# Kernel optimization log

Hardware: AMD Instinct MI355X
Metric: run time of the kernel (lower is better)

## Reference

```python
import jax, jax.numpy as jnp
import numpy as np

N = 100000      # nodes
E = 1600000     # edges (before self-loops)
DIN = 256
D = 128         # dmid == dout
L = 4           # n_layers
ALPHA = 0.5
THETA = 1.0
EPS = 1e-5      # pyg LayerNorm default eps


def setup_inputs() -> dict:
    key = jax.random.key(0)
    ks = jax.random.split(key, 6)
    x = jax.random.normal(ks[0], (N, DIN), jnp.float32)
    edge_index = jax.random.randint(ks[1], (2, E), 0, N)
    lin1_w = jax.random.normal(ks[2], (D, DIN), jnp.float32) * (1.0 / np.sqrt(DIN))
    lin1_b = jnp.zeros((D,), jnp.float32)
    w1 = jax.random.normal(ks[3], (L, D, D), jnp.float32) * (1.0 / np.sqrt(D))
    w2 = jax.random.normal(ks[4], (L, D, D), jnp.float32) * (1.0 / np.sqrt(D))
    norm_w = jnp.ones((D,), jnp.float32)
    norm_b = jnp.zeros((D,), jnp.float32)
    return {"x": x, "edge_index": edge_index, "lin1_w": lin1_w, "lin1_b": lin1_b,
            "w1": w1, "w2": w2, "norm_w": norm_w, "norm_b": norm_b}


def reference(x, edge_index, lin1_w, lin1_b, w1, w2, norm_w, norm_b):
    # --- gcn_norm: add self-loops, symmetric degree normalization ---
    sl = jnp.arange(N)
    row = jnp.concatenate([edge_index[0], sl])  # sources
    col = jnp.concatenate([edge_index[1], sl])  # targets (aggregation index)
    deg = jax.ops.segment_sum(jnp.ones(row.shape[0], jnp.float32), col, num_segments=N)
    dis = jax.lax.rsqrt(deg)  # deg >= 1 thanks to self-loops
    enorm = dis[row] * dis[col]  # [E+N]

    # --- f_0 = relu(lin1(x)); prev_h = 0 so x_0 arg == f_0 ---
    f0 = jax.nn.relu(x @ lin1_w.T + lin1_b)  # [N, D]
    x0 = ALPHA * f0
    f = f0

    for i in range(L):
        beta = float(np.log(THETA / (i + 1) + 1.0))
        # sparse neighbor aggregation: h = A_hat @ f
        h = jax.ops.segment_sum(f[row] * enorm[:, None], col, num_segments=N)
        h = h * (1.0 - ALPHA)
        # shared_weights=False: two separate identity/weight mixes
        out = ((1.0 - beta) * h + beta * (h @ w1[i])
               + (1.0 - beta) * x0 + beta * (x0 @ w2[i]))
        # pyg LayerNorm mode='graph', batch=None: normalize over all nodes+channels
        m = out.mean()
        s = jnp.sqrt(jnp.mean((out - m) ** 2))
        out = (out - m) / (s + EPS) * norm_w + norm_b
        f = jax.nn.relu(out)

    # dmid == dout -> lin2 is Identity
    return jax.nn.relu(f)
```

## Files before the change

kernel.cpp:

```cpp
#include <hip/hip_runtime.h>
#include <math.h>

constexpr int N    = 100000;
constexpr int E    = 1600000;
constexpr int DIN  = 256;
constexpr int D    = 128;
constexpr int L    = 4;
constexpr float EPS = 1e-5f;
constexpr int NPP  = 12500;

typedef __attribute__((ext_vector_type(8))) short bf16x8;
typedef __attribute__((ext_vector_type(4))) float f32x4;
typedef __attribute__((ext_vector_type(2))) float f32x2;

__device__ inline ushort f2b(float f) {
    uint u = __float_as_uint(f);
    uint r = u + 0x7fffu + ((u >> 16) & 1u);
    return (ushort)(r >> 16);
}
__device__ inline float b2f(ushort b) { return __uint_as_float(((uint)b) << 16); }


__global__ void k_count(const int* __restrict__ col, int* __restrict__ cnt) {
    int i = blockIdx.x * 256 + threadIdx.x;
    if (i * 2 + 1 < E) {
        int2 cc = ((const int2*)col)[i];
        atomicAdd(&cnt[cc.x], 1);
        atomicAdd(&cnt[cc.y], 1);
    } else if (i * 2 < E) {
        atomicAdd(&cnt[col[i * 2]], 1);
    }
}

__global__ void k_dis(const int* __restrict__ cnt, float* __restrict__ dis) {
    int n = blockIdx.x * 256 + threadIdx.x;
    if (n < N) dis[n] = rsqrtf((float)cnt[n] + 1.0f);
}

__global__ void k_blocksum(const int* __restrict__ cnt, int* __restrict__ bsum) {
    __shared__ int s[256];
    int base = blockIdx.x * 1024;
    int t = threadIdx.x;
    int a = 0;
    for (int j = 0; j < 4; j++) {
        int idx = base + t * 4 + j;
        if (idx < N) a += cnt[idx];
    }
    s[t] = a; __syncthreads();
    for (int off = 128; off > 0; off >>= 1) {
        if (t < off) s[t] += s[t + off];
        __syncthreads();
    }
    if (t == 0) bsum[blockIdx.x] = s[0];
}

__global__ void k_scan(int* __restrict__ bsum, int nb) {
    __shared__ int s[128];
    int t = threadIdx.x;
    int v = (t < nb) ? bsum[t] : 0;
    s[t] = v; __syncthreads();
    for (int off = 1; off < 128; off <<= 1) {
        int x = (t >= off) ? s[t - off] : 0;
        __syncthreads();
        s[t] += x;
        __syncthreads();
    }
    if (t < nb) bsum[t] = s[t] - v;
}

__global__ void k_offsets(const int* __restrict__ cnt, const int* __restrict__ bsum,
                          int* __restrict__ offs) {
    __shared__ int ls[256];
    int b = blockIdx.x, t = threadIdx.x;
    int base = b * 1024;
    int v[4]; int s = 0;
    for (int j = 0; j < 4; j++) {
        int idx = base + t * 4 + j;
        v[j] = (idx < N) ? cnt[idx] : 0;
        s += v[j];
    }
    ls[t] = s; __syncthreads();
    for (int off = 1; off < 256; off <<= 1) {
        int x = (t >= off) ? ls[t - off] : 0;
        __syncthreads();
        ls[t] += x;
        __syncthreads();
    }
    int excl = ((t == 0) ? 0 : ls[t - 1]) + bsum[b];
    for (int j = 0; j < 4; j++) {
        int idx = base + t * 4 + j;
        if (idx < N) offs[idx] = excl;
        excl += v[j];
        if (idx == N - 1) offs[N] = excl;
    }
}

__global__ void k_scatter(const int* __restrict__ row, const int* __restrict__ col,
                          const float* __restrict__ dis, int* __restrict__ cur,
                          int2* __restrict__ csr) {
    int part = blockIdx.x & 7;
    int base = ((blockIdx.x >> 3) * 256 + threadIdx.x) * 4;
    if (base >= E) return;
    int4 c4 = *(const int4*)(col + base);
    int4 r4 = *(const int4*)(row + base);
    int cs[4] = {c4.x, c4.y, c4.z, c4.w};
    int rs[4] = {r4.x, r4.y, r4.z, r4.w};
    #pragma unroll
    for (int j = 0; j < 4; j++) {
        if (cs[j] / NPP == part) {
            int pos = atomicAdd(&cur[cs[j]], 1);
            csr[pos] = make_int2(rs[j], __float_as_int(dis[rs[j]] * dis[cs[j]]));
        }
    }
}


__global__ void k_prep_w(const float* __restrict__ lin1_w, const float* __restrict__ w1,
                         const float* __restrict__ w2, float4 betas,
                         ushort* __restrict__ wb0, ushort* __restrict__ wbc) {
    int i = blockIdx.x * 256 + threadIdx.x;
    if (i < D * DIN) wb0[i] = f2b(lin1_w[i]);
    if (i < L * D * 256) {
        int l = i >> 15, r = i & 32767, d = r >> 8, k = r & 255;
        float beta = (l == 0) ? betas.x : (l == 1) ? betas.y : (l == 2) ? betas.z : betas.w;
        float v;
        if (k < 128) v = beta * w1[l * 16384 + k * 128 + d] + ((k == d) ? (1.f - beta) : 0.f);
        else { int kk = k - 128; v = beta * w2[l * 16384 + kk * 128 + d] + ((kk == d) ? (1.f - beta) : 0.f); }
        wbc[l * 32768 + d * 256 + k] = f2b(v);
    }
}


__global__ __launch_bounds__(512, 2) void k_f0_mfma(const float* __restrict__ x,
        const ushort* __restrict__ wb, const float* __restrict__ bias,
        ushort* __restrict__ f_bf, ushort* __restrict__ x0_bf) {
    __shared__ uint4 Bl[4096];
    int t = threadIdx.x;
    #pragma unroll
    for (int it = 0; it < 8; it++) {
        int d = it * 512 + t, c = d >> 5, ck = d & 31;
        Bl[c * 32 + (ck ^ (c & 7))] = ((const uint4*)wb)[d];
    }
    __syncthreads();

    int wv = t >> 6, lane = t & 63;
    int l16 = lane & 15, g16 = lane >> 4;
    int row0 = (blockIdx.x * 8 + wv) * 16;
    if (row0 >= N) return;

    const uint4* xb = (const uint4*)(x + (size_t)(row0 + l16) * 256);
    uint4 xr[16];
    #pragma unroll
    for (int ks = 0; ks < 8; ks++) {
        xr[2 * ks]     = xb[ks * 8 + g16 * 2];
        xr[2 * ks + 1] = xb[ks * 8 + g16 * 2 + 1];
    }

    f32x4 acc[8];
    #pragma unroll
    for (int n = 0; n < 8; n++) acc[n] = f32x4{0.f, 0.f, 0.f, 0.f};

    #pragma unroll
    for (int ks = 0; ks < 8; ks++) {
        float4 lo = *(const float4*)&xr[2 * ks];
        float4 hi = *(const float4*)&xr[2 * ks + 1];
        uint4 p;
        p.x = (uint)f2b(lo.x) | ((uint)f2b(lo.y) << 16);
        p.y = (uint)f2b(lo.z) | ((uint)f2b(lo.w) << 16);
        p.z = (uint)f2b(hi.x) | ((uint)f2b(hi.y) << 16);
        p.w = (uint)f2b(hi.z) | ((uint)f2b(hi.w) << 16);
        bf16x8 a = *(bf16x8*)&p;
        int xo = (ks * 4 + g16) ^ (l16 & 7);
        const char* bp = (const char*)Bl + l16 * 512 + xo * 16;
        #pragma unroll
        for (int n = 0; n < 8; n++) {
            bf16x8 b = *(const bf16x8*)(bp + n * 8192);
            acc[n] = __builtin_amdgcn_mfma_f32_16x16x32_bf16(a, b, acc[n], 0, 0, 0);
        }
    }

    float bc[8];
    #pragma unroll
    for (int n = 0; n < 8; n++) bc[n] = bias[n * 16 + l16];
    #pragma unroll
    for (int j = 0; j < 4; j++) {
        int gr = row0 + g16 * 4 + j;
        #pragma unroll
        for (int n = 0; n < 8; n++) {
            float r = fmaxf(acc[n][j] + bc[n], 0.f);
            size_t o = (size_t)gr * 128 + n * 16 + l16;
            f_bf[o] = f2b(r);
            x0_bf[o] = f2b(0.5f * r);
        }
    }
}


__global__ __launch_bounds__(512, 2) void k_combine_mfma(const ushort* __restrict__ g_bf,
        const ushort* __restrict__ x0_bf, const ushort* __restrict__ wb,
        ushort* __restrict__ h_bf, float* __restrict__ sr) {
    __shared__ uint4 Bl[4096];
    __shared__ float red1[512];
    __shared__ float red2[512];
    int t = threadIdx.x;
    #pragma unroll
    for (int it = 0; it < 8; it++) {
        int d = it * 512 + t, c = d >> 5, ck = d & 31;
        Bl[c * 32 + (ck ^ (c & 7))] = ((const uint4*)wb)[d];
    }
    __syncthreads();

    int wv = t >> 6, lane = t & 63;
    int l16 = lane & 15, g16 = lane >> 4;
    int row0 = (blockIdx.x * 8 + wv) * 16;
    bool active = row0 < N;

    f32x4 acc[8];
    #pragma unroll
    for (int n = 0; n < 8; n++) acc[n] = f32x4{0.f, 0.f, 0.f, 0.f};

    if (active) {
        const uint4* ga = (const uint4*)(g_bf  + (size_t)(row0 + l16) * 128);
        const uint4* xa = (const uint4*)(x0_bf + (size_t)(row0 + l16) * 128);
        uint4 ar[8];
        #pragma unroll
        for (int ks = 0; ks < 4; ks++) ar[ks]     = ga[ks * 4 + g16];
        #pragma unroll
        for (int ks = 0; ks < 4; ks++) ar[ks + 4] = xa[ks * 4 + g16];

        #pragma unroll
        for (int ks = 0; ks < 8; ks++) {
            bf16x8 a = *(bf16x8*)&ar[ks];
            int xo = (ks * 4 + g16) ^ (l16 & 7);
            const char* bp = (const char*)Bl + l16 * 512 + xo * 16;
            #pragma unroll
            for (int n = 0; n < 8; n++) {
                bf16x8 b = *(const bf16x8*)(bp + n * 8192);
                acc[n] = __builtin_amdgcn_mfma_f32_16x16x32_bf16(a, b, acc[n], 0, 0, 0);
            }
        }
    }

    float sum = 0.f, sq = 0.f;
    if (active) {
        #pragma unroll
        for (int n = 0; n < 8; n++)
            #pragma unroll
            for (int j = 0; j < 4; j++) { float v = acc[n][j]; sum += v; sq += v * v; }
        #pragma unroll
        for (int j = 0; j < 4; j++) {
            int gr = row0 + g16 * 4 + j;
            #pragma unroll
            for (int n = 0; n < 8; n++)
                h_bf[(size_t)gr * 128 + n * 16 + l16] = f2b(acc[n][j]);
        }
    }

    red1[t] = sum; red2[t] = sq; __syncthreads();
    for (int off = 256; off > 0; off >>= 1) {
        if (t < off) { red1[t] += red1[t + off]; red2[t] += red2[t + off]; }
        __syncthreads();
    }
    if (t == 0) { atomicAdd(&sr[0], red1[0]); atomicAdd(&sr[1], red2[0]); }
}


template <int AFFINE>
__global__ __launch_bounds__(256) void k_agg(const ushort* __restrict__ src,
        const int* __restrict__ offs, const int2* __restrict__ csr,
        const float* __restrict__ dis, const float* __restrict__ sr,
        const float* __restrict__ nw, const float* __restrict__ nb,
        ushort* __restrict__ g_bf) {
    int node = blockIdx.x * 4 + (threadIdx.x >> 6);
    if (node >= N) return;
    int lane = threadIdx.x & 63;
    int q = lane >> 4, cl = lane & 15;
    const uint4* fu = (const uint4*)src;

    f32x2 sc[4], sh[4];
    if constexpr (AFFINE) {
        const float inv_n = 1.0f / ((float)N * (float)D);
        float m = sr[0] * inv_n;
        float var = fmaxf(sr[1] * inv_n - m * m, 0.f);
        float inv = 1.0f / (sqrtf(var) + EPS);
        #pragma unroll
        for (int p = 0; p < 4; p++) {
            float w0 = nw[cl * 8 + 2 * p], w1 = nw[cl * 8 + 2 * p + 1];
            sc[p] = f32x2{inv * w0, inv * w1};
            sh[p] = f32x2{nb[cl * 8 + 2 * p]     - m * inv * w0,
                          nb[cl * 8 + 2 * p + 1] - m * inv * w1};
        }
    }

    f32x2 a2[4];
    #pragma unroll
    for (int p = 0; p < 4; p++) a2[p] = f32x2{0.f, 0.f};

    auto acc8 = [&](float val, uint4 rv) {
        uint uu[4] = {rv.x, rv.y, rv.z, rv.w};
        f32x2 v2 = {val, val};
        #pragma unroll
        for (int p = 0; p < 4; p++) {
            f32x2 c;
            c.x = __uint_as_float(uu[p] << 16);
            c.y = __uint_as_float(uu[p] & 0xffff0000u);
            if constexpr (AFFINE) {
                c = __builtin_elementwise_fma(c, sc[p], sh[p]);
                c = __builtin_elementwise_max(c, f32x2{0.f, 0.f});
            }
            a2[p] = __builtin_elementwise_fma(v2, c, a2[p]);
        }
    };

    float dv = dis[node];
    acc8((q == 0) ? dv * dv : 0.f, fu[(size_t)node * 16 + cl]);

    int end = offs[node + 1];
    int i = offs[node] + q * 4;
    if (i < end) {
        int2 rA[4], rB[4];
        uint4 wA[4];
        #pragma unroll
        for (int s = 0; s < 4; s++) rA[s] = csr[min(i + s, end - 1)];
        #pragma unroll
        for (int s = 0; s < 4; s++) wA[s] = fu[(size_t)rA[s].x * 16 + cl];
        #pragma unroll
        for (int s = 0; s < 4; s++) rB[s] = csr[min(i + 16 + s, end - 1)];
        while (i + 16 < end) {
            uint4 wB[4];
            #pragma unroll
            for (int s = 0; s < 4; s++) wB[s] = fu[(size_t)rB[s].x * 16 + cl];
            int2 rC[4];
            #pragma unroll
            for (int s = 0; s < 4; s++) rC[s] = csr[min(i + 32 + s, end - 1)];
            #pragma unroll
            for (int s = 0; s < 4; s++) acc8(__int_as_float(rA[s].y), wA[s]);
            #pragma unroll
            for (int s = 0; s < 4; s++) { rA[s] = rB[s]; wA[s] = wB[s]; rB[s] = rC[s]; }
            i += 16;
        }
        #pragma unroll
        for (int s = 0; s < 4; s++) {
            float v = (i + s < end) ? __int_as_float(rA[s].y) : 0.f;
            acc8(v, wA[s]);
        }
    }

    #pragma unroll
    for (int p = 0; p < 4; p++) {
        a2[p].x += __shfl_xor(a2[p].x, 16, 64);
        a2[p].x += __shfl_xor(a2[p].x, 32, 64);
        a2[p].y += __shfl_xor(a2[p].y, 16, 64);
        a2[p].y += __shfl_xor(a2[p].y, 32, 64);
    }
    if (q == 0) {
        uint4 o;
        o.x = (uint)f2b(0.5f * a2[0].x) | ((uint)f2b(0.5f * a2[0].y) << 16);
        o.y = (uint)f2b(0.5f * a2[1].x) | ((uint)f2b(0.5f * a2[1].y) << 16);
        o.z = (uint)f2b(0.5f * a2[2].x) | ((uint)f2b(0.5f * a2[2].y) << 16);
        o.w = (uint)f2b(0.5f * a2[3].x) | ((uint)f2b(0.5f * a2[3].y) << 16);
        ((uint4*)g_bf)[(size_t)node * 16 + cl] = o;
    }
}


__global__ void k_ln_final(const ushort* __restrict__ ob, const float* __restrict__ sr,
                           const float* __restrict__ nw, const float* __restrict__ nb,
                           float* __restrict__ fout) {
    int i = blockIdx.x * 256 + threadIdx.x;
    if (i >= N * 16) return;
    const float inv_n = 1.0f / ((float)N * (float)D);
    float m = sr[0] * inv_n;
    float var = fmaxf(sr[1] * inv_n - m * m, 0.f);
    float inv = 1.0f / (sqrtf(var) + EPS);
    uint4 v = ((const uint4*)ob)[i];
    int c = (i & 15) * 8;
    uint vv[4] = {v.x, v.y, v.z, v.w};
    float r[8];
    #pragma unroll
    for (int qd = 0; qd < 4; qd++) {
        float lo = b2f((ushort)(vv[qd] & 0xffff));
        float hi = b2f((ushort)(vv[qd] >> 16));
        r[2 * qd]     = fmaxf((lo - m) * inv * nw[c + 2 * qd]     + nb[c + 2 * qd], 0.f);
        r[2 * qd + 1] = fmaxf((hi - m) * inv * nw[c + 2 * qd + 1] + nb[c + 2 * qd + 1], 0.f);
    }
    float4 o0 = {r[0], r[1], r[2], r[3]};
    float4 o1 = {r[4], r[5], r[6], r[7]};
    ((float4*)fout)[2 * i] = o0;
    ((float4*)fout)[2 * i + 1] = o1;
}


extern "C" void kernel_launch(void* const* d_in, const int* in_sizes, int n_in,
                              void* d_out, int out_size, void* d_ws, size_t ws_size,
                              hipStream_t stream) {
    const float* x      = (const float*)d_in[0];
    const int*   ei     = (const int*)d_in[1];
    const float* lin1_w = (const float*)d_in[2];
    const float* lin1_b = (const float*)d_in[3];
    const float* w1     = (const float*)d_in[4];
    const float* w2     = (const float*)d_in[5];
    const float* nw     = (const float*)d_in[6];
    const float* nb     = (const float*)d_in[7];
    const int* row = ei;
    const int* col = ei + E;
    float* fout = (float*)d_out;

    char* ws = (char*)d_ws;
    size_t off0 = 0;
    auto alloc = [&](size_t bytes) -> char* {
        char* p = ws + off0;
        off0 = (off0 + bytes + 255) & ~(size_t)255;
        return p;
    };
    ushort* f_bf    = (ushort*)alloc((size_t)N * D * 2);
    ushort* x0_bf   = (ushort*)alloc((size_t)N * D * 2);
    ushort* g_bf    = (ushort*)alloc((size_t)N * D * 2);
    ushort* h_bf    = (ushort*)alloc((size_t)N * D * 2);
    float*  dis     = (float*) alloc((size_t)N * 4);
    int*    cnt     = (int*)   alloc((size_t)N * 4);
    int*    offs    = (int*)   alloc((size_t)(N + 1) * 4);
    int*    cur     = (int*)   alloc((size_t)N * 4);
    int*    bsum    = (int*)   alloc((size_t)128 * 4);
    int2*   csr     = (int2*)  alloc((size_t)E * 8);
    float*  stats   = (float*) alloc(64);
    ushort* wb0     = (ushort*)alloc((size_t)D * DIN * 2);
    ushort* wbc     = (ushort*)alloc((size_t)L * D * 256 * 2);

    hipMemsetAsync(cnt, 0, (size_t)N * 4, stream);
    hipMemsetAsync(stats, 0, 64, stream);

    k_count<<<(E / 2 + 255) / 256, 256, 0, stream>>>(col, cnt);
    k_dis<<<(N + 255) / 256, 256, 0, stream>>>(cnt, dis);
    int nbk = (N + 1023) / 1024;
    k_blocksum<<<nbk, 256, 0, stream>>>(cnt, bsum);
    k_scan<<<1, 128, 0, stream>>>(bsum, nbk);
    k_offsets<<<nbk, 256, 0, stream>>>(cnt, bsum, offs);
    hipMemcpyAsync(cur, offs, (size_t)N * 4, hipMemcpyDeviceToDevice, stream);
    int echunks = (E / 4 + 255) / 256;
    k_scatter<<<echunks * 8, 256, 0, stream>>>(row, col, dis, cur, csr);

    float4 betas;
    betas.x = logf(1.0f / 1.0f + 1.0f);
    betas.y = logf(1.0f / 2.0f + 1.0f);
    betas.z = logf(1.0f / 3.0f + 1.0f);
    betas.w = logf(1.0f / 4.0f + 1.0f);
    k_prep_w<<<(L * D * 256 + 255) / 256, 256, 0, stream>>>(lin1_w, w1, w2, betas, wb0, wbc);

    int GB = (N / 16 + 7) / 8;
    k_f0_mfma<<<GB, 512, 0, stream>>>(x, wb0, lin1_b, f_bf, x0_bf);

    int AGB = (N + 3) / 4;
    for (int i = 0; i < L; i++) {
        if (i == 0)
            k_agg<0><<<AGB, 256, 0, stream>>>(f_bf, offs, csr, dis, nullptr, nw, nb, g_bf);
        else
            k_agg<1><<<AGB, 256, 0, stream>>>(h_bf, offs, csr, dis, stats + 2 * (i - 1),
                                              nw, nb, g_bf);
        k_combine_mfma<<<GB, 512, 0, stream>>>(g_bf, x0_bf, wbc + (size_t)i * D * 256,
                                               h_bf, stats + 2 * i);
    }
    k_ln_final<<<(N * 16 + 255) / 256, 256, 0, stream>>>(h_bf, stats + 6, nw, nb, fout);
}
```

Before: 591.4 us.

## Replace partitioned CSR scatter with two-pass bin-then-scatter via staging buffer

The old scatter re-read all edges 8 times, with each pass scattering only the edges whose target falls in one node partition. It is replaced by two passes. First, edges are binned into 256 coarse target-node bins through a shared-memory histogram and staged contiguously. Second, each bin is scattered into the final CSR, so the random writes stay within a localized region of the CSR. This removes the 8x redundant edge reads and improves write locality, at the cost of an extra staging buffer of E int2 entries and one more pass over it.

```diff
diff --git a/kernel.cpp b/kernel.cpp
--- a/kernel.cpp
+++ b/kernel.cpp
@@ -7,7 +7,8 @@
 constexpr int D    = 128;
 constexpr int L    = 4;
 constexpr float EPS = 1e-5f;
-constexpr int NPP  = 12500;
+constexpr int NBIN = 256;
+constexpr int BINW = 391;
 
 typedef __attribute__((ext_vector_type(8))) short bf16x8;
 typedef __attribute__((ext_vector_type(4))) float f32x4;
@@ -95,22 +96,50 @@
     }
 }
 
-__global__ void k_scatter(const int* __restrict__ row, const int* __restrict__ col,
-                          const float* __restrict__ dis, int* __restrict__ cur,
-                          int2* __restrict__ csr) {
-    int part = blockIdx.x & 7;
-    int base = ((blockIdx.x >> 3) * 256 + threadIdx.x) * 4;
-    if (base >= E) return;
-    int4 c4 = *(const int4*)(col + base);
-    int4 r4 = *(const int4*)(row + base);
-    int cs[4] = {c4.x, c4.y, c4.z, c4.w};
-    int rs[4] = {r4.x, r4.y, r4.z, r4.w};
-    #pragma unroll
-    for (int j = 0; j < 4; j++) {
-        if (cs[j] / NPP == part) {
-            int pos = atomicAdd(&cur[cs[j]], 1);
-            csr[pos] = make_int2(rs[j], __float_as_int(dis[rs[j]] * dis[cs[j]]));
-        }
+__global__ void k_bininit(const int* __restrict__ offs, int* __restrict__ bcur) {
+    int t = threadIdx.x;
+    if (t < NBIN) bcur[t] = offs[min(t * BINW, N)];
+}
+
+__global__ __launch_bounds__(256) void k_bin(const int* __restrict__ row,
+        const int* __restrict__ col, int* __restrict__ bcur, int2* __restrict__ stag) {
+    __shared__ int hist[NBIN];
+    __shared__ int base[NBIN];
+    int t = threadIdx.x;
+    int e0 = blockIdx.x * 2048;
+    if (t < NBIN) hist[t] = 0;
+    __syncthreads();
+    int r[8], c[8], li[8], bn[8];
+    #pragma unroll
+    for (int j = 0; j < 8; j++) {
+        int e = e0 + j * 256 + t;
+        if (e < E) {
+            c[j] = col[e]; r[j] = row[e];
+            bn[j] = c[j] / BINW;
+            li[j] = atomicAdd(&hist[bn[j]], 1);
+        }
+    }
+    __syncthreads();
+    if (t < NBIN) base[t] = hist[t] ? atomicAdd(&bcur[t], hist[t]) : 0;
+    __syncthreads();
+    #pragma unroll
+    for (int j = 0; j < 8; j++) {
+        int e = e0 + j * 256 + t;
+        if (e < E) stag[base[bn[j]] + li[j]] = make_int2(r[j], c[j]);
+    }
+}
+
+__global__ __launch_bounds__(256) void k_unbin(const int2* __restrict__ stag,
+        const int* __restrict__ offs, const float* __restrict__ dis,
+        int* __restrict__ cur, int2* __restrict__ csr) {
+    int b = blockIdx.x >> 2, part = blockIdx.x & 3;
+    int s = offs[min(b * BINW, N)];
+    int e = offs[min((b + 1) * BINW, N)];
+    for (int i = s + part * 256 + threadIdx.x; i < e; i += 1024) {
+        int2 rc = stag[i];
+        float v = dis[rc.x] * dis[rc.y];
+        int pos = atomicAdd(&cur[rc.y], 1);
+        csr[pos] = make_int2(rc.x, __float_as_int(v));
     }
 }
 
@@ -422,6 +451,8 @@
     int*    offs    = (int*)   alloc((size_t)(N + 1) * 4);
     int*    cur     = (int*)   alloc((size_t)N * 4);
     int*    bsum    = (int*)   alloc((size_t)128 * 4);
+    int*    bcur    = (int*)   alloc((size_t)NBIN * 4);
+    int2*   stag    = (int2*)  alloc((size_t)E * 8);
     int2*   csr     = (int2*)  alloc((size_t)E * 8);
     float*  stats   = (float*) alloc(64);
     ushort* wb0     = (ushort*)alloc((size_t)D * DIN * 2);
@@ -436,9 +467,10 @@
     k_blocksum<<<nbk, 256, 0, stream>>>(cnt, bsum);
     k_scan<<<1, 128, 0, stream>>>(bsum, nbk);
     k_offsets<<<nbk, 256, 0, stream>>>(cnt, bsum, offs);
+    k_bininit<<<1, 256, 0, stream>>>(offs, bcur);
     hipMemcpyAsync(cur, offs, (size_t)N * 4, hipMemcpyDeviceToDevice, stream);
-    int echunks = (E / 4 + 255) / 256;
-    k_scatter<<<echunks * 8, 256, 0, stream>>>(row, col, dis, cur, csr);
+    k_bin<<<(E + 2047) / 2048, 256, 0, stream>>>(row, col, bcur, stag);
+    k_unbin<<<NBIN * 4, 256, 0, stream>>>(stag, offs, dis, cur, csr);
 
     float4 betas;
     betas.x = logf(1.0f / 1.0f + 1.0f);
```

After: 591.7 us. About the same (+0.0%).
